# Kernel optimization log

Hardware: AMD Instinct MI355X
Metric: run time of the kernel (lower is better)

Reference implementation:

```python
import jax, jax.numpy as jnp
import numpy as np

N = 100000        # nodes
E = 1600000       # edges
NFEAT = 500
NHID = [256, 128]
NCLASS = 40
K = 10
ALPHA = 0.1


def setup_inputs() -> dict:
    key = jax.random.key(0)
    ks = jax.random.split(key, 9)
    x = jax.random.normal(ks[0], (N, NFEAT), dtype=jnp.float32)
    edge_index = jax.random.randint(ks[1], (2, E), 0, N, dtype=jnp.int32)
    dims = [NFEAT] + NHID + [NCLASS]
    # Linear params (PyTorch convention: W is [out, in])
    W0 = jax.random.normal(ks[2], (dims[1], dims[0]), jnp.float32) / np.sqrt(dims[0])
    b0 = jnp.zeros((dims[1],), jnp.float32)
    W1 = jax.random.normal(ks[3], (dims[2], dims[1]), jnp.float32) / np.sqrt(dims[1])
    b1 = jnp.zeros((dims[2],), jnp.float32)
    W2 = jax.random.normal(ks[4], (dims[3], dims[2]), jnp.float32) / np.sqrt(dims[2])
    b2 = jnp.zeros((dims[3],), jnp.float32)
    return {"x": x, "edge_index": edge_index,
            "W0": W0, "b0": b0, "W1": W1, "b1": b1, "W2": W2, "b2": b2}


def reference(x, edge_index, W0, b0, W1, b1, W2, b2):
    # MLP encoder: ReLU after every Linear (dropout is identity in eval mode)
    h = x
    for W, b in ((W0, b0), (W1, b1), (W2, b2)):
        h = jax.nn.relu(h @ W.T + b)   # [N, out]

    # --- APPNP propagation with GCN normalization (self-loops added) ---
    loops = jnp.arange(N, dtype=edge_index.dtype)
    src = jnp.concatenate([edge_index[0], loops])  # [E+N]
    dst = jnp.concatenate([edge_index[1], loops])  # [E+N]
    deg = jnp.zeros((N,), h.dtype).at[dst].add(jnp.ones_like(dst, h.dtype))
    dinv = jax.lax.rsqrt(deg)                      # deg >= 1 due to self-loops
    norm = dinv[src] * dinv[dst]                   # [E+N]

    h0 = h
    for _ in range(K):
        msg = h[src] * norm[:, None]               # gather + scale, [E+N, C]
        agg = jnp.zeros_like(h).at[dst].add(msg)   # scatter-add, [N, C]
        h = (1.0 - ALPHA) * agg + ALPHA * h0       # teleport fusion
    return h
```

## Files before the change

### kernel.cpp

```cpp
#include <hip/hip_runtime.h>

#define NN 100000
#define EE 1600000
#define KITER 10

typedef __attribute__((ext_vector_type(8))) short s16x8;
typedef __attribute__((ext_vector_type(4))) float f32x4;

__device__ __forceinline__ short f2bf(float f) {
    union { float f; unsigned u; } v; v.f = f;
    unsigned r = v.u + 0x7FFFu + ((v.u >> 16) & 1u);
    return (short)(r >> 16);
}
__device__ __forceinline__ float bf2f(short s) {
    return __uint_as_float((unsigned)(unsigned short)s << 16);
}

__device__ __forceinline__ void gload_lds16(const void* g, void* l) {
    __builtin_amdgcn_global_load_lds(
        (const __attribute__((address_space(1))) void*)g,
        (__attribute__((address_space(3))) void*)l, 16, 0, 0);
}

template<int KSTEPS, bool OUT_BF16>
__global__ __launch_bounds__(256)
void mfma_gemm(const short* __restrict__ A, int lda, const short* __restrict__ B,
               const float* __restrict__ bias, int nbias,
               void* __restrict__ Cout, short* __restrict__ CoutHi, int ldc,
               int ncols_store, int nrows, float* __restrict__ C2)
{
    __shared__ short ldsA[128 * 32];
    __shared__ short ldsB[128 * 32];
    const int t    = threadIdx.x;
    const int lane = t & 63;
    const int wid  = t >> 6;
    const int rowBase = blockIdx.y * 128;
    const int colBase = blockIdx.x * 128;
    const int wrow = (wid >> 1) * 64;
    const int wcol = (wid & 1) * 64;

    const int q  = t & 3;
    const int rl = t >> 2;

    f32x4 acc[4][4] = {};
    const int KPB = KSTEPS * 32;

    for (int ks = 0; ks < KSTEPS; ++ks) {
        const int k0 = ks * 32;

        #pragma unroll
        for (int i = 0; i < 2; ++i) {
            const short* srcB = B + (size_t)(colBase + rl + i * 64) * KPB + k0 + q * 8;
            gload_lds16(srcB, &ldsB[wid * 512 + i * 2048]);
        }
        #pragma unroll
        for (int i = 0; i < 2; ++i) {
            int grow = rowBase + rl + i * 64; if (grow > NN - 1) grow = NN - 1;
            const short* srcA = A + (size_t)grow * lda + k0 + q * 8;
            gload_lds16(srcA, &ldsA[wid * 512 + i * 2048]);
        }

        __syncthreads();

        {
            const int kb = lane >> 4;
            const int l16 = lane & 15;
            s16x8 a[4], b[4];
            #pragma unroll
            for (int m = 0; m < 4; ++m)
                a[m] = *(const s16x8*)&ldsA[(wrow + m * 16 + l16) * 32 + kb * 8];
            #pragma unroll
            for (int n = 0; n < 4; ++n)
                b[n] = *(const s16x8*)&ldsB[(wcol + n * 16 + l16) * 32 + kb * 8];
            #pragma unroll
            for (int m = 0; m < 4; ++m)
                #pragma unroll
                for (int n = 0; n < 4; ++n)
                    acc[m][n] = __builtin_amdgcn_mfma_f32_16x16x32_bf16(
                        a[m], b[n], acc[m][n], 0, 0, 0);
        }

        __syncthreads();
    }

    const int crow0 = (lane >> 4) * 4;
    const int ccol  = lane & 15;
    #pragma unroll
    for (int n = 0; n < 4; ++n) {
        int col = colBase + wcol + n * 16 + ccol;
        float bv = (col < nbias) ? bias[col] : 0.f;
        #pragma unroll
        for (int m = 0; m < 4; ++m) {
            #pragma unroll
            for (int j = 0; j < 4; ++j) {
                int row = rowBase + wrow + m * 16 + crow0 + j;
                if (row >= nrows) continue;
                float v = acc[m][n][j] + bv;
                v = fmaxf(v, 0.f);
                if (col < ncols_store) {
                    if (OUT_BF16) {
                        short bvv = f2bf(v);
                        if (CoutHi) {
                            if (col < 32) ((short*)Cout)[(size_t)row * 32 + col] = bvv;
                            else          CoutHi[(size_t)row * 8 + (col - 32)] = bvv;
                        } else {
                            ((short*)Cout)[(size_t)row * ldc + col] = bvv;
                        }
                    } else {
                        ((float*)Cout)[(size_t)row * ldc + col] = v;
                    }
                    if (C2) C2[(size_t)row * ldc + col] = v;
                }
            }
        }
    }
}

__global__ void convert_x_kernel(const float* __restrict__ in, short* __restrict__ out) {
    int idx = blockIdx.x * blockDim.x + threadIdx.x;
    if (idx >= (NN * 500) / 8) return;
    const float4* in4 = (const float4*)in;
    float4 a = in4[(size_t)idx * 2];
    float4 b = in4[(size_t)idx * 2 + 1];
    s16x8 s;
    s[0]=f2bf(a.x); s[1]=f2bf(a.y); s[2]=f2bf(a.z); s[3]=f2bf(a.w);
    s[4]=f2bf(b.x); s[5]=f2bf(b.y); s[6]=f2bf(b.z); s[7]=f2bf(b.w);
    *(s16x8*)&out[(size_t)idx * 8] = s;
}

__global__ void convert_w_kernel(const float* __restrict__ in, short* __restrict__ out,
                                 int R, int C, int Rp, int Cp) {
    int idx = blockIdx.x * blockDim.x + threadIdx.x;
    if (idx >= Rp * Cp) return;
    int r = idx / Cp, c = idx - r * Cp;
    float v = (r < R && c < C) ? in[r * C + c] : 0.f;
    out[idx] = f2bf(v);
}

__global__ void deg_init_kernel(int* deg, int n) {
    int i = blockIdx.x * blockDim.x + threadIdx.x;
    if (i < n) deg[i] = 1;
}
__global__ void deg_count_kernel(const int* __restrict__ dst, int* deg, int e) {
    int i = blockIdx.x * blockDim.x + threadIdx.x;
    if (i < e) atomicAdd(&deg[dst[i]], 1);
}
__global__ void dinv_kernel(const int* __restrict__ deg, float* __restrict__ dinv,
                            float* __restrict__ dinv2, int n) {
    int i = blockIdx.x * blockDim.x + threadIdx.x;
    if (i < n) {
        float d = (float)deg[i];
        dinv[i] = rsqrtf(d);
        dinv2[i] = 1.0f / d;
    }
}
__global__ __launch_bounds__(256)
void scan1_kernel(const int* __restrict__ deg, int* __restrict__ row_ptr,
                  int* __restrict__ blockSums, int n) {
    __shared__ int sdata[256];
    const int base = blockIdx.x * 2048;
    const int t = threadIdx.x;
    int local[8];
    int s = 0;
    #pragma unroll
    for (int i = 0; i < 8; ++i) {
        int idx = base + t * 8 + i;
        int c = (idx < n) ? (deg[idx] - 1) : 0;
        local[i] = s;
        s += c;
    }
    sdata[t] = s;
    __syncthreads();
    for (int off = 1; off < 256; off <<= 1) {
        int v = (t >= off) ? sdata[t - off] : 0;
        __syncthreads();
        sdata[t] += v;
        __syncthreads();
    }
    int excl = (t == 0) ? 0 : sdata[t - 1];
    #pragma unroll
    for (int i = 0; i < 8; ++i) {
        int idx = base + t * 8 + i;
        if (idx < n) row_ptr[idx] = excl + local[i];
    }
    if (t == 255) blockSums[blockIdx.x] = sdata[255];
}
__global__ void scan2_kernel(int* blockSums, int nb) {
    if (threadIdx.x == 0 && blockIdx.x == 0) {
        int s = 0;
        for (int i = 0; i < nb; ++i) { int v = blockSums[i]; blockSums[i] = s; s += v; }
    }
}
__global__ void scan3_kernel(int* __restrict__ row_ptr, int* __restrict__ cursor,
                             const int* __restrict__ blockSums, int n, int e) {
    int i = blockIdx.x * blockDim.x + threadIdx.x;
    if (i < n) {
        int v = row_ptr[i] + blockSums[i >> 11];
        row_ptr[i] = v;
        cursor[i] = v;
    }
    if (i == 0) row_ptr[n] = e;
}
__global__ void fill_csr_kernel(const int* __restrict__ src, const int* __restrict__ dst,
                                const float* __restrict__ dinv, int* cursor,
                                int2* __restrict__ pairs, int e) {
    int i = blockIdx.x * blockDim.x + threadIdx.x;
    if (i < e) {
        int s = src[i], d = dst[i];
        int pos = atomicAdd(&cursor[d], 1);
        float nv = dinv[s] * dinv[d];
        pairs[pos] = make_int2(s, __float_as_int(nv));
    }
}

__global__ __launch_bounds__(320)
void prop_split_kernel(const short* __restrict__ hin_lo, const short* __restrict__ hin_hi,
                       const float* __restrict__ h0f,
                       const int* __restrict__ rowp, const int2* __restrict__ pairs,
                       const float* __restrict__ dinv2,
                       short* __restrict__ hout_lo, short* __restrict__ hout_hi,
                       float* __restrict__ outF, int n)
{
    const int t = threadIdx.x;
    const int vl = t / 5;
    const int f = t - vl * 5;
    const int v = blockIdx.x * 64 + vl;
    if (v >= n) return;

    const bool isLo = (f < 4);
    const short* gbase = isLo ? hin_lo : hin_hi;
    const int gmul = isLo ? 32 : 8;
    const int goff = isLo ? f * 8 : 0;

    float acc[8];
    {
        const float dv = dinv2[v];
        s16x8 s = *(const s16x8*)(gbase + (size_t)v * gmul + goff);
        #pragma unroll
        for (int j = 0; j < 8; ++j) acc[j] = dv * bf2f(s[j]);
    }

    int e = rowp[v];
    const int e1 = rowp[v + 1];

    for (; e + 8 <= e1; e += 8) {
        int2 p0 = pairs[e],     p1 = pairs[e + 1], p2 = pairs[e + 2], p3 = pairs[e + 3];
        int2 p4 = pairs[e + 4], p5 = pairs[e + 5], p6 = pairs[e + 6], p7 = pairs[e + 7];
        s16x8 g0 = *(const s16x8*)(gbase + (size_t)p0.x * gmul + goff);
        s16x8 g1 = *(const s16x8*)(gbase + (size_t)p1.x * gmul + goff);
        s16x8 g2 = *(const s16x8*)(gbase + (size_t)p2.x * gmul + goff);
        s16x8 g3 = *(const s16x8*)(gbase + (size_t)p3.x * gmul + goff);
        s16x8 g4 = *(const s16x8*)(gbase + (size_t)p4.x * gmul + goff);
        s16x8 g5 = *(const s16x8*)(gbase + (size_t)p5.x * gmul + goff);
        s16x8 g6 = *(const s16x8*)(gbase + (size_t)p6.x * gmul + goff);
        s16x8 g7 = *(const s16x8*)(gbase + (size_t)p7.x * gmul + goff);
        float w0 = __int_as_float(p0.y), w1 = __int_as_float(p1.y);
        float w2 = __int_as_float(p2.y), w3 = __int_as_float(p3.y);
        float w4 = __int_as_float(p4.y), w5 = __int_as_float(p5.y);
        float w6 = __int_as_float(p6.y), w7 = __int_as_float(p7.y);
        #pragma unroll
        for (int j = 0; j < 8; ++j) acc[j] = fmaf(w0, bf2f(g0[j]), acc[j]);
        #pragma unroll
        for (int j = 0; j < 8; ++j) acc[j] = fmaf(w1, bf2f(g1[j]), acc[j]);
        #pragma unroll
        for (int j = 0; j < 8; ++j) acc[j] = fmaf(w2, bf2f(g2[j]), acc[j]);
        #pragma unroll
        for (int j = 0; j < 8; ++j) acc[j] = fmaf(w3, bf2f(g3[j]), acc[j]);
        #pragma unroll
        for (int j = 0; j < 8; ++j) acc[j] = fmaf(w4, bf2f(g4[j]), acc[j]);
        #pragma unroll
        for (int j = 0; j < 8; ++j) acc[j] = fmaf(w5, bf2f(g5[j]), acc[j]);
        #pragma unroll
        for (int j = 0; j < 8; ++j) acc[j] = fmaf(w6, bf2f(g6[j]), acc[j]);
        #pragma unroll
        for (int j = 0; j < 8; ++j) acc[j] = fmaf(w7, bf2f(g7[j]), acc[j]);
    }
    for (; e < e1; ++e) {
        int2 p = pairs[e];
        s16x8 g = *(const s16x8*)(gbase + (size_t)p.x * gmul + goff);
        float w = __int_as_float(p.y);
        #pragma unroll
        for (int j = 0; j < 8; ++j) acc[j] = fmaf(w, bf2f(g[j]), acc[j]);
    }

    const float* h0p = h0f + (size_t)v * 40 + (isLo ? f * 8 : 32);
    float o[8];
    #pragma unroll
    for (int j = 0; j < 8; ++j) o[j] = fmaf(0.9f, acc[j], 0.1f * h0p[j]);

    if (outF) {
        float4* op = (float4*)(outF + (size_t)v * 40 + (isLo ? f * 8 : 32));
        op[0] = make_float4(o[0], o[1], o[2], o[3]);
        op[1] = make_float4(o[4], o[5], o[6], o[7]);
    } else {
        s16x8 s;
        #pragma unroll
        for (int j = 0; j < 8; ++j) s[j] = f2bf(o[j]);
        short* obase = isLo ? hout_lo : hout_hi;
        *(s16x8*)(obase + (size_t)v * gmul + goff) = s;
    }
}

extern "C" void kernel_launch(void* const* d_in, const int* in_sizes, int n_in,
                              void* d_out, int out_size, void* d_ws, size_t ws_size,
                              hipStream_t stream) {
    const float* x  = (const float*)d_in[0];
    const int* ei   = (const int*)d_in[1];
    const float* W0 = (const float*)d_in[2];
    const float* b0 = (const float*)d_in[3];
    const float* W1 = (const float*)d_in[4];
    const float* b1 = (const float*)d_in[5];
    const float* W2 = (const float*)d_in[6];
    const float* b2 = (const float*)d_in[7];
    float* out = (float*)d_out;
    char* ws = (char*)d_ws;

    const int* src = ei;
    const int* dst = ei + EE;

    short* xb   = (short*)(ws);
    short* h1b  = (short*)(ws + 100000000);
    short* W0b  = (short*)(ws + 151200000);
    short* W1b  = (short*)(ws + 151462144);
    short* W2b  = (short*)(ws + 151527680);

    short* h2b  = (short*)(ws);
    short* h0lo = (short*)(ws + 25600000);
    short* h0hi = (short*)(ws + 32000000);
    float* h0f  = (float*)(ws + 33600000);
    short* hAlo = (short*)(ws + 49600000);
    short* hAhi = (short*)(ws + 56000000);
    short* hBlo = (short*)(ws + 57600000);
    short* hBhi = (short*)(ws + 64000000);

    int2*  pairs= (int2*) (ws + 100000000);
    int*   deg  = (int*)  (ws + 112800000);
    float* dinv = (float*)(ws + 113200000);
    float* dnv2 = (float*)(ws + 113600000);
    int*   rowp = (int*)  (ws + 114000000);
    int*   curs = (int*)  (ws + 114400008);
    int*   bsum = (int*)  (ws + 114800008);
    (void)ws_size; (void)in_sizes; (void)n_in; (void)out_size;

    convert_x_kernel<<<((NN * 500 / 8) + 255) / 256, 256, 0, stream>>>(x, xb);
    convert_w_kernel<<<(256 * 512 + 255) / 256, 256, 0, stream>>>(W0, W0b, 256, 500, 256, 512);
    convert_w_kernel<<<(128 * 256 + 255) / 256, 256, 0, stream>>>(W1, W1b, 128, 256, 128, 256);
    convert_w_kernel<<<(128 * 128 + 255) / 256, 256, 0, stream>>>(W2, W2b, 40, 128, 128, 128);

    const int NBLK = (NN + 127) / 128;
    mfma_gemm<16, true ><<<dim3(2, NBLK), 256, 0, stream>>>(
        xb, 500, W0b, b0, 256, (void*)h1b, nullptr, 256, 256, NN, nullptr);
    mfma_gemm<8,  true ><<<dim3(1, NBLK), 256, 0, stream>>>(
        h1b, 256, W1b, b1, 128, (void*)h2b, nullptr, 128, 128, NN, nullptr);
    mfma_gemm<4,  true ><<<dim3(1, NBLK), 256, 0, stream>>>(
        h2b, 128, W2b, b2, 40, (void*)h0lo, h0hi, 40, 40, NN, h0f);

    {
        int nb_n = (NN + 255) / 256;
        int nb_e = (EE + 255) / 256;
        deg_init_kernel<<<nb_n, 256, 0, stream>>>(deg, NN);
        deg_count_kernel<<<nb_e, 256, 0, stream>>>(dst, deg, EE);
        dinv_kernel<<<nb_n, 256, 0, stream>>>(deg, dinv, dnv2, NN);
        int nb_scan = (NN + 2047) / 2048;
        scan1_kernel<<<nb_scan, 256, 0, stream>>>(deg, rowp, bsum, NN);
        scan2_kernel<<<1, 64, 0, stream>>>(bsum, nb_scan);
        scan3_kernel<<<nb_n, 256, 0, stream>>>(rowp, curs, bsum, NN, EE);
        fill_csr_kernel<<<nb_e, 256, 0, stream>>>(src, dst, dinv, curs, pairs, EE);
    }

    {
        dim3 blk(320);
        dim3 grd((NN + 63) / 64);
        const short* hlo = h0lo;
        const short* hhi = h0hi;
        for (int it = 0; it < KITER; ++it) {
            short* olo = (it & 1) ? hBlo : hAlo;
            short* ohi = (it & 1) ? hBhi : hAhi;
            float* fin = (it == KITER - 1) ? out : nullptr;
            prop_split_kernel<<<grd, blk, 0, stream>>>(
                hlo, hhi, h0f, rowp, pairs, dnv2, olo, ohi, fin, NN);
            hlo = olo; hhi = ohi;
        }
    }
}
```

Measured before the change: 843.9 us.

## Split propagation into separate lo and hi feature kernels

Replaces the fused 5-lanes-per-node propagation kernel with two kernels per iteration. One handles the 32 low features using 4 lanes per node, and the other handles the 8 high features using 1 thread per node. This removes the divide-by-5 indexing and the divergent lo/hi branching inside a wavefront. In exchange, every iteration reads the CSR pairs and row pointers twice and launches twice as many kernels.

```diff
diff --git a/kernel.cpp b/kernel.cpp
--- a/kernel.cpp
+++ b/kernel.cpp
@@ -213,29 +213,22 @@
     }
 }
 
-__global__ __launch_bounds__(320)
-void prop_split_kernel(const short* __restrict__ hin_lo, const short* __restrict__ hin_hi,
-                       const float* __restrict__ h0f,
-                       const int* __restrict__ rowp, const int2* __restrict__ pairs,
-                       const float* __restrict__ dinv2,
-                       short* __restrict__ hout_lo, short* __restrict__ hout_hi,
-                       float* __restrict__ outF, int n)
+__global__ __launch_bounds__(256)
+void prop_lo_kernel(const short* __restrict__ hin_lo, const float* __restrict__ h0f,
+                    const int* __restrict__ rowp, const int2* __restrict__ pairs,
+                    const float* __restrict__ dinv2,
+                    short* __restrict__ hout_lo, float* __restrict__ outF, int n)
 {
     const int t = threadIdx.x;
-    const int vl = t / 5;
-    const int f = t - vl * 5;
+    const int vl = t >> 2;
+    const int f = t & 3;
     const int v = blockIdx.x * 64 + vl;
     if (v >= n) return;
-
-    const bool isLo = (f < 4);
-    const short* gbase = isLo ? hin_lo : hin_hi;
-    const int gmul = isLo ? 32 : 8;
-    const int goff = isLo ? f * 8 : 0;
 
     float acc[8];
     {
         const float dv = dinv2[v];
-        s16x8 s = *(const s16x8*)(gbase + (size_t)v * gmul + goff);
+        s16x8 s = *(const s16x8*)(hin_lo + (size_t)v * 32 + f * 8);
         #pragma unroll
         for (int j = 0; j < 8; ++j) acc[j] = dv * bf2f(s[j]);
     }
@@ -246,14 +239,14 @@
     for (; e + 8 <= e1; e += 8) {
         int2 p0 = pairs[e],     p1 = pairs[e + 1], p2 = pairs[e + 2], p3 = pairs[e + 3];
         int2 p4 = pairs[e + 4], p5 = pairs[e + 5], p6 = pairs[e + 6], p7 = pairs[e + 7];
-        s16x8 g0 = *(const s16x8*)(gbase + (size_t)p0.x * gmul + goff);
-        s16x8 g1 = *(const s16x8*)(gbase + (size_t)p1.x * gmul + goff);
-        s16x8 g2 = *(const s16x8*)(gbase + (size_t)p2.x * gmul + goff);
-        s16x8 g3 = *(const s16x8*)(gbase + (size_t)p3.x * gmul + goff);
-        s16x8 g4 = *(const s16x8*)(gbase + (size_t)p4.x * gmul + goff);
-        s16x8 g5 = *(const s16x8*)(gbase + (size_t)p5.x * gmul + goff);
-        s16x8 g6 = *(const s16x8*)(gbase + (size_t)p6.x * gmul + goff);
-        s16x8 g7 = *(const s16x8*)(gbase + (size_t)p7.x * gmul + goff);
+        s16x8 g0 = *(const s16x8*)(hin_lo + (size_t)p0.x * 32 + f * 8);
+        s16x8 g1 = *(const s16x8*)(hin_lo + (size_t)p1.x * 32 + f * 8);
+        s16x8 g2 = *(const s16x8*)(hin_lo + (size_t)p2.x * 32 + f * 8);
+        s16x8 g3 = *(const s16x8*)(hin_lo + (size_t)p3.x * 32 + f * 8);
+        s16x8 g4 = *(const s16x8*)(hin_lo + (size_t)p4.x * 32 + f * 8);
+        s16x8 g5 = *(const s16x8*)(hin_lo + (size_t)p5.x * 32 + f * 8);
+        s16x8 g6 = *(const s16x8*)(hin_lo + (size_t)p6.x * 32 + f * 8);
+        s16x8 g7 = *(const s16x8*)(hin_lo + (size_t)p7.x * 32 + f * 8);
         float w0 = __int_as_float(p0.y), w1 = __int_as_float(p1.y);
         float w2 = __int_as_float(p2.y), w3 = __int_as_float(p3.y);
         float w4 = __int_as_float(p4.y), w5 = __int_as_float(p5.y);
@@ -277,27 +270,103 @@
     }
     for (; e < e1; ++e) {
         int2 p = pairs[e];
-        s16x8 g = *(const s16x8*)(gbase + (size_t)p.x * gmul + goff);
+        s16x8 g = *(const s16x8*)(hin_lo + (size_t)p.x * 32 + f * 8);
         float w = __int_as_float(p.y);
         #pragma unroll
         for (int j = 0; j < 8; ++j) acc[j] = fmaf(w, bf2f(g[j]), acc[j]);
     }
 
-    const float* h0p = h0f + (size_t)v * 40 + (isLo ? f * 8 : 32);
+    const float* h0p = h0f + (size_t)v * 40 + f * 8;
     float o[8];
     #pragma unroll
     for (int j = 0; j < 8; ++j) o[j] = fmaf(0.9f, acc[j], 0.1f * h0p[j]);
 
     if (outF) {
-        float4* op = (float4*)(outF + (size_t)v * 40 + (isLo ? f * 8 : 32));
+        float4* op = (float4*)(outF + (size_t)v * 40 + f * 8);
         op[0] = make_float4(o[0], o[1], o[2], o[3]);
         op[1] = make_float4(o[4], o[5], o[6], o[7]);
     } else {
         s16x8 s;
         #pragma unroll
         for (int j = 0; j < 8; ++j) s[j] = f2bf(o[j]);
-        short* obase = isLo ? hout_lo : hout_hi;
-        *(s16x8*)(obase + (size_t)v * gmul + goff) = s;
+        *(s16x8*)(hout_lo + (size_t)v * 32 + f * 8) = s;
+    }
+}
+
+__global__ __launch_bounds__(256)
+void prop_hi_kernel(const short* __restrict__ hin_hi, const float* __restrict__ h0f,
+                    const int* __restrict__ rowp, const int2* __restrict__ pairs,
+                    const float* __restrict__ dinv2,
+                    short* __restrict__ hout_hi, float* __restrict__ outF, int n)
+{
+    const int v = blockIdx.x * 256 + threadIdx.x;
+    if (v >= n) return;
+
+    float acc[8];
+    {
+        const float dv = dinv2[v];
+        s16x8 s = *(const s16x8*)(hin_hi + (size_t)v * 8);
+        #pragma unroll
+        for (int j = 0; j < 8; ++j) acc[j] = dv * bf2f(s[j]);
+    }
+
+    int e = rowp[v];
+    const int e1 = rowp[v + 1];
+
+    for (; e + 8 <= e1; e += 8) {
+        int2 p0 = pairs[e],     p1 = pairs[e + 1], p2 = pairs[e + 2], p3 = pairs[e + 3];
+        int2 p4 = pairs[e + 4], p5 = pairs[e + 5], p6 = pairs[e + 6], p7 = pairs[e + 7];
+        s16x8 g0 = *(const s16x8*)(hin_hi + (size_t)p0.x * 8);
+        s16x8 g1 = *(const s16x8*)(hin_hi + (size_t)p1.x * 8);
+        s16x8 g2 = *(const s16x8*)(hin_hi + (size_t)p2.x * 8);
+        s16x8 g3 = *(const s16x8*)(hin_hi + (size_t)p3.x * 8);
+        s16x8 g4 = *(const s16x8*)(hin_hi + (size_t)p4.x * 8);
+        s16x8 g5 = *(const s16x8*)(hin_hi + (size_t)p5.x * 8);
+        s16x8 g6 = *(const s16x8*)(hin_hi + (size_t)p6.x * 8);
+        s16x8 g7 = *(const s16x8*)(hin_hi + (size_t)p7.x * 8);
+        float w0 = __int_as_float(p0.y), w1 = __int_as_float(p1.y);
+        float w2 = __int_as_float(p2.y), w3 = __int_as_float(p3.y);
+        float w4 = __int_as_float(p4.y), w5 = __int_as_float(p5.y);
+        float w6 = __int_as_float(p6.y), w7 = __int_as_float(p7.y);
+        #pragma unroll
+        for (int j = 0; j < 8; ++j) acc[j] = fmaf(w0, bf2f(g0[j]), acc[j]);
+        #pragma unroll
+        for (int j = 0; j < 8; ++j) acc[j] = fmaf(w1, bf2f(g1[j]), acc[j]);
+        #pragma unroll
+        for (int j = 0; j < 8; ++j) acc[j] = fmaf(w2, bf2f(g2[j]), acc[j]);
+        #pragma unroll
+        for (int j = 0; j < 8; ++j) acc[j] = fmaf(w3, bf2f(g3[j]), acc[j]);
+        #pragma unroll
+        for (int j = 0; j < 8; ++j) acc[j] = fmaf(w4, bf2f(g4[j]), acc[j]);
+        #pragma unroll
+        for (int j = 0; j < 8; ++j) acc[j] = fmaf(w5, bf2f(g5[j]), acc[j]);
+        #pragma unroll
+        for (int j = 0; j < 8; ++j) acc[j] = fmaf(w6, bf2f(g6[j]), acc[j]);
+        #pragma unroll
+        for (int j = 0; j < 8; ++j) acc[j] = fmaf(w7, bf2f(g7[j]), acc[j]);
+    }
+    for (; e < e1; ++e) {
+        int2 p = pairs[e];
+        s16x8 g = *(const s16x8*)(hin_hi + (size_t)p.x * 8);
+        float w = __int_as_float(p.y);
+        #pragma unroll
+        for (int j = 0; j < 8; ++j) acc[j] = fmaf(w, bf2f(g[j]), acc[j]);
+    }
+
+    const float* h0p = h0f + (size_t)v * 40 + 32;
+    float o[8];
+    #pragma unroll
+    for (int j = 0; j < 8; ++j) o[j] = fmaf(0.9f, acc[j], 0.1f * h0p[j]);
+
+    if (outF) {
+        float4* op = (float4*)(outF + (size_t)v * 40 + 32);
+        op[0] = make_float4(o[0], o[1], o[2], o[3]);
+        op[1] = make_float4(o[4], o[5], o[6], o[7]);
+    } else {
+        s16x8 s;
+        #pragma unroll
+        for (int j = 0; j < 8; ++j) s[j] = f2bf(o[j]);
+        *(s16x8*)(hout_hi + (size_t)v * 8) = s;
     }
 }
 
@@ -369,16 +438,18 @@
     }
 
     {
-        dim3 blk(320);
-        dim3 grd((NN + 63) / 64);
+        dim3 gLo((NN + 63) / 64);
+        dim3 gHi((NN + 255) / 256);
         const short* hlo = h0lo;
         const short* hhi = h0hi;
         for (int it = 0; it < KITER; ++it) {
             short* olo = (it & 1) ? hBlo : hAlo;
             short* ohi = (it & 1) ? hBhi : hAhi;
             float* fin = (it == KITER - 1) ? out : nullptr;
-            prop_split_kernel<<<grd, blk, 0, stream>>>(
-                hlo, hhi, h0f, rowp, pairs, dnv2, olo, ohi, fin, NN);
+            prop_lo_kernel<<<gLo, 256, 0, stream>>>(
+                hlo, h0f, rowp, pairs, dnv2, olo, fin, NN);
+            prop_hi_kernel<<<gHi, 256, 0, stream>>>(
+                hhi, h0f, rowp, pairs, dnv2, ohi, fin, NN);
             hlo = olo; hhi = ohi;
         }
     }
```

Result: faster. 823.7 us (-2.4%).
